# Kernel tuning notes

Hardware: AMD Instinct MI355X
Metric: run time of the kernel (lower is better)

The kernel has to match this reference:

```python
import jax, jax.numpy as jnp
import numpy as np

B, M = 512, 256
IN1, IN2, IN3 = 20000, 15000, 20000


def setup_inputs() -> dict:
    key = jax.random.key(0)
    ks = jax.random.split(key, 16)
    s1, s2, s3, s4 = 1.0 / np.sqrt(IN1), 1.0 / np.sqrt(IN2), 1.0 / np.sqrt(IN3), 1.0 / np.sqrt(4 * M)
    return {
        "expression": jax.random.normal(ks[0], (B, IN1), jnp.float32),
        "mutation": jax.random.uniform(ks[1], (B, IN2), jnp.float32),
        "cna": jax.random.normal(ks[2], (B, IN3), jnp.float32),
        "We_x": jax.random.normal(ks[3], (M, IN1), jnp.float32) * s1,
        "We_y": jax.random.normal(ks[4], (M, IN1), jnp.float32) * s1,
        "Wm_x": jax.random.normal(ks[5], (M, IN2), jnp.float32) * s2,
        "Wm_y": jax.random.normal(ks[6], (M, IN2), jnp.float32) * s2,
        "Wc_x": jax.random.normal(ks[7], (M, IN3), jnp.float32) * s3,
        "Wc_y": jax.random.normal(ks[8], (M, IN3), jnp.float32) * s3,
        "W3e": jax.random.normal(ks[9], (1, 4 * M), jnp.float32) * s4,
        "b3e": jnp.zeros((1,), jnp.float32),
        "W3m": jax.random.normal(ks[10], (1, 4 * M), jnp.float32) * s4,
        "b3m": jnp.zeros((1,), jnp.float32),
        "W3c": jax.random.normal(ks[11], (1, 4 * M), jnp.float32) * s4,
        "b3c": jnp.zeros((1,), jnp.float32),
    }


def reference(expression, mutation, cna, We_x, We_y, Wm_x, Wm_y, Wc_x, Wc_y,
              W3e, b3e, W3m, b3m, W3c, b3c):
    def proj(x, Wx, Wy):  # (B,F) -> (B,2,M)
        return jnp.stack([x @ Wx.T, x @ Wy.T], axis=1)

    def l2norm(t):  # normalize over the 2-row axis, like torch.norm(dim=1,keepdim=True)
        return t / jnp.linalg.norm(t, axis=1, keepdims=True)

    e = l2norm(proj(expression, We_x, We_y))
    m = l2norm(proj(mutation, Wm_x, Wm_y))
    c = l2norm(proj(cna, Wc_x, Wc_y))

    energy = lambda a, b: jnp.einsum('bkm,bkn->bmn', a, b)  # (B,M,M), k=2
    E_em, E_ec, E_mc = energy(e, m), energy(e, c), energy(m, c)

    att_em = jax.nn.softmax(E_em, axis=1)                     # softmax over dim1
    att_ec = jax.nn.softmax(E_ec, axis=1)
    att_me = jnp.swapaxes(jax.nn.softmax(E_em, axis=-1), 1, 2)
    att_mc = jax.nn.softmax(E_mc, axis=-1)                    # double permute cancels
    att_ce = jnp.swapaxes(jax.nn.softmax(E_ec, axis=-1), 1, 2)
    att_cm = jnp.swapaxes(jax.nn.softmax(E_mc, axis=-1), 1, 2)

    w = lambda x, a: jnp.einsum('bkm,bmn->bkn', x, a)  # (B,2,M)
    e_feat = jnp.concatenate([w(e, att_em), w(e, att_ec)], axis=1).reshape(-1, 4 * e.shape[-1])
    m_feat = jnp.concatenate([w(m, att_me), w(m, att_mc)], axis=1).reshape(-1, 4 * e.shape[-1])
    c_feat = jnp.concatenate([w(c, att_ce), w(c, att_cm)], axis=1).reshape(-1, 4 * e.shape[-1])

    head = lambda f, W, b: jnp.squeeze(jax.nn.sigmoid(f @ W.T + b))
    return head(e_feat, W3e, b3e), head(m_feat, W3m, b3m), head(c_feat, W3c, b3c)
```

## Files before the change

### kernel.cpp

```cpp
#include <hip/hip_runtime.h>
#include <hip/hip_bf16.h>

typedef short short8 __attribute__((ext_vector_type(8)));
typedef float float4v __attribute__((ext_vector_type(4)));

#define TK 32
#define MAXSPLIT 20
#define APAD 40

__device__ __forceinline__ unsigned int pack2bf(float a, float b) {
    unsigned int r;
    asm("v_cvt_pk_bf16_f32 %0, %1, %2" : "=v"(r) : "v"(a), "v"(b));
    return r;
}

__global__ __launch_bounds__(512, 2) void gemm_kernel(
    const float* __restrict__ Ae, const float* __restrict__ Am, const float* __restrict__ Ac,
    const float* __restrict__ Wex, const float* __restrict__ Wey,
    const float* __restrict__ Wmx, const float* __restrict__ Wmy,
    const float* __restrict__ Wcx, const float* __restrict__ Wcy,
    float* __restrict__ part, int nsplit)
{
    int nb = gridDim.x;
    int per = nb >> 3;
    int bid = blockIdx.x;
    int job = (bid & 7) * per + (bid >> 3);

    int mod = job / (4 * nsplit);
    int rem = job - mod * 4 * nsplit;
    int split = rem >> 2;
    int t2 = rem & 3;
    int ti = t2 >> 1, tj = t2 & 1;

    const float* A; const float* Wx; const float* Wy; int K;
    if (mod == 0)      { A = Ae; Wx = Wex; Wy = Wey; K = 20000; }
    else if (mod == 1) { A = Am; Wx = Wmx; Wy = Wmy; K = 15000; }
    else               { A = Ac; Wx = Wcx; Wy = Wcy; K = 20000; }

    int chunk = ((K + nsplit * TK - 1) / (nsplit * TK)) * TK;
    int kstart = split * chunk;
    int kend = kstart + chunk; if (kend > K) kend = K;
    int nstep = (kend - kstart + TK - 1) / TK;

    const float* Abase = A + (size_t)(ti * 256) * K;
    const float* Wbase = (tj == 0) ? Wx : Wy;

    __shared__ unsigned short As[2][256][APAD];
    __shared__ unsigned short Bs[2][256][APAD];

    int tid = threadIdx.x;
    int lane = tid & 63, w = tid >> 6;
    int wr = (w & 3) * 64;
    int wc = (w >> 2) * 128;
    int q = lane >> 4, r16 = lane & 15, q8 = q * 8;

    int ra0 = tid >> 3;
    int ca  = (tid & 7) * 4;

    float4v ar[4], br[4];
    auto loadAB = [&](int k0) {
        int k = k0 + ca; if (k > K - 4) k = K - 4;
        #pragma unroll
        for (int i = 0; i < 4; ++i) {
            ar[i] = *(const float4v*)(Abase + (size_t)(ra0 + i * 64) * K + k);
            br[i] = *(const float4v*)(Wbase + (size_t)(ra0 + i * 64) * K + k);
        }
    };
    auto storeAB = [&](int buf, int k0, bool tail) {
        bool kill = tail && (k0 + ca >= kend);
        #pragma unroll
        for (int i = 0; i < 4; ++i) {
            float4v va = ar[i], vb = br[i];
            if (kill) { va = (float4v){0.f,0.f,0.f,0.f}; vb = (float4v){0.f,0.f,0.f,0.f}; }
            uint2 pa, pb;
            pa.x = pack2bf(va[0], va[1]);
            pa.y = pack2bf(va[2], va[3]);
            pb.x = pack2bf(vb[0], vb[1]);
            pb.y = pack2bf(vb[2], vb[3]);
            *(uint2*)&As[buf][ra0 + i * 64][ca] = pa;
            *(uint2*)&Bs[buf][ra0 + i * 64][ca] = pb;
        }
    };

    float4v acc[4][8];
    #pragma unroll
    for (int a = 0; a < 4; ++a)
        #pragma unroll
        for (int b = 0; b < 8; ++b)
            acc[a][b] = (float4v){0.f, 0.f, 0.f, 0.f};

    auto computeStep = [&](int buf) {
        short8 fa[4], fb[8];
        #pragma unroll
        for (int a = 0; a < 4; ++a)
            fa[a] = *(const short8*)&As[buf][wr + a * 16 + r16][q8];
        #pragma unroll
        for (int b = 0; b < 8; ++b)
            fb[b] = *(const short8*)&Bs[buf][wc + b * 16 + r16][q8];
        #pragma unroll
        for (int a = 0; a < 4; ++a)
            #pragma unroll
            for (int b = 0; b < 8; ++b)
                acc[a][b] = __builtin_amdgcn_mfma_f32_16x16x32_bf16(fa[a], fb[b], acc[a][b], 0, 0, 0);
    };

    loadAB(kstart);
    storeAB(0, kstart, kstart + TK > kend);

    for (int s = 0; s < nstep; ++s) {
        int cur = s & 1;
        int k1 = kstart + (s + 1) * TK;
        bool more = (s + 1 < nstep);
        if (more) loadAB(k1);
        __syncthreads();
        computeStep(cur);
        if (more) storeAB(cur ^ 1, k1, k1 + TK > kend);
    }

    float* pbase = part + (size_t)((mod * 4 + t2) * nsplit + split) * 65536;
    #pragma unroll
    for (int a = 0; a < 4; ++a)
        #pragma unroll
        for (int b = 0; b < 8; ++b)
            #pragma unroll
            for (int r = 0; r < 4; ++r) {
                int row = wr + a * 16 + q * 4 + r;
                int col = wc + b * 16 + r16;
                pbase[row * 256 + col] = acc[a][b][r];
            }
}

__global__ void reduce_kernel(const float* __restrict__ part, float* __restrict__ P,
                              float* __restrict__ headacc, int nsplit)
{
    int gid = blockIdx.x * 256 + threadIdx.x;
    if (gid < 1536) headacc[gid] = 0.f;
    int mod = gid >> 18;
    int rem = gid & 262143;
    int b = rem >> 9, j = rem & 511;
    int ti = b >> 8, r = b & 255, tj = j >> 8, c = j & 255;
    int t2 = ti * 2 + tj;
    const float* src = part + (size_t)((mod * 4 + t2) * nsplit) * 65536 + r * 256 + c;
    float s = 0.f;
    for (int k = 0; k < nsplit; ++k) s += src[(size_t)k * 65536];
    P[gid] = s;
}

__global__ __launch_bounds__(256) void pairs_kernel(
    const float* __restrict__ P, float* __restrict__ headacc,
    const float* __restrict__ W3e, const float* __restrict__ W3m, const float* __restrict__ W3c)
{
    int b = blockIdx.x / 3, pair = blockIdx.x % 3;
    int t = threadIdx.x;
    __shared__ float2 Pn[256], Qn[256];
    __shared__ float Rinv[256];
    __shared__ float red[4];

    int pm = (pair == 2) ? 1 : 0;
    int qm = (pair == 0) ? 1 : 2;
    const float* prow = P + pm * 262144 + b * 512;
    const float* qrow = P + qm * 262144 + b * 512;

    float px = prow[t], py = prow[256 + t];
    float ip = rsqrtf(px * px + py * py);
    Pn[t] = (float2){px * ip, py * ip};
    float qx = qrow[t], qy = qrow[256 + t];
    float iq = rsqrtf(qx * qx + qy * qy);
    Qn[t] = (float2){qx * iq, qy * iq};
    __syncthreads();

    const float L2E = 1.4426950408889634f;

    float pxr = Pn[t].x * L2E, pyr = Pn[t].y * L2E;
    float rs = 0.f, rqx = 0.f, rqy = 0.f;
    #pragma unroll 4
    for (int j = 0; j < 256; ++j) {
        float2 qv = Qn[j];
        float x = exp2f(fmaf(pyr, qv.y, pxr * qv.x));
        rs += x;
        rqx = fmaf(qv.x, x, rqx);
        rqy = fmaf(qv.y, x, rqy);
    }
    float rinv = 1.f / rs;
    Rinv[t] = rinv;
    float Fq0 = rqx * rinv, Fq1 = rqy * rinv;

    const float* WR; int hR, offR;
    if (pair == 0)      { WR = W3m; hR = 1; offR = 0; }
    else if (pair == 1) { WR = W3c; hR = 2; offR = 0; }
    else                { WR = W3c; hR = 2; offR = 512; }
    float v = Fq0 * WR[offR + t] + Fq1 * WR[offR + 256 + t];
    #pragma unroll
    for (int o = 32; o > 0; o >>= 1) v += __shfl_down(v, o, 64);
    if ((t & 63) == 0) red[t >> 6] = v;
    __syncthreads();
    if (t == 0) atomicAdd(&headacc[b * 3 + hR], red[0] + red[1] + red[2] + red[3]);
    __syncthreads();

    float qxr = Qn[t].x * L2E, qyr = Qn[t].y * L2E;
    float cs = 0.f, cpx = 0.f, cpy = 0.f;
    if (pair < 2) {
        #pragma unroll 4
        for (int i = 0; i < 256; ++i) {
            float2 pv = Pn[i];
            float x = exp2f(fmaf(qyr, pv.y, qxr * pv.x));
            cs += x;
            cpx = fmaf(pv.x, x, cpx);
            cpy = fmaf(pv.y, x, cpy);
        }
        float ci = 1.f / cs;
        cpx *= ci; cpy *= ci;
    } else {
        #pragma unroll 4
        for (int i = 0; i < 256; ++i) {
            float2 pv = Pn[i];
            float x = exp2f(fmaf(qyr, pv.y, qxr * pv.x)) * Rinv[i];
            cpx = fmaf(pv.x, x, cpx);
            cpy = fmaf(pv.y, x, cpy);
        }
    }
    const float* WC; int hC, offC;
    if (pair == 0)      { WC = W3e; hC = 0; offC = 0; }
    else if (pair == 1) { WC = W3e; hC = 0; offC = 512; }
    else                { WC = W3m; hC = 1; offC = 512; }
    float v2 = cpx * WC[offC + t] + cpy * WC[offC + 256 + t];
    #pragma unroll
    for (int o = 32; o > 0; o >>= 1) v2 += __shfl_down(v2, o, 64);
    if ((t & 63) == 0) red[t >> 6] = v2;
    __syncthreads();
    if (t == 0) atomicAdd(&headacc[b * 3 + hC], red[0] + red[1] + red[2] + red[3]);
}

__global__ void head_kernel(const float* __restrict__ headacc,
                            const float* __restrict__ b3e, const float* __restrict__ b3m,
                            const float* __restrict__ b3c, float* __restrict__ out)
{
    int i = blockIdx.x * 256 + threadIdx.x;
    if (i >= 1536) return;
    int h = i >> 9, b = i & 511;
    float bias = (h == 0) ? b3e[0] : (h == 1) ? b3m[0] : b3c[0];
    float z = headacc[b * 3 + h] + bias;
    out[i] = 1.f / (1.f + __expf(-z));
}

extern "C" void kernel_launch(void* const* d_in, const int* in_sizes, int n_in,
                              void* d_out, int out_size, void* d_ws, size_t ws_size,
                              hipStream_t stream) {
    const float* Ae  = (const float*)d_in[0];
    const float* Am  = (const float*)d_in[1];
    const float* Ac  = (const float*)d_in[2];
    const float* Wex = (const float*)d_in[3];
    const float* Wey = (const float*)d_in[4];
    const float* Wmx = (const float*)d_in[5];
    const float* Wmy = (const float*)d_in[6];
    const float* Wcx = (const float*)d_in[7];
    const float* Wcy = (const float*)d_in[8];
    const float* W3e = (const float*)d_in[9];
    const float* b3e = (const float*)d_in[10];
    const float* W3m = (const float*)d_in[11];
    const float* b3m = (const float*)d_in[12];
    const float* W3c = (const float*)d_in[13];
    const float* b3c = (const float*)d_in[14];

    size_t fixed = (size_t)786432 * 4 + 1536 * 4;
    int nsplit = 2;
    if (ws_size > fixed) {
        size_t avail = (ws_size - fixed) / ((size_t)12 * 65536 * 4);
        nsplit = (avail < MAXSPLIT) ? (int)avail : MAXSPLIT;
        if (nsplit < 2) nsplit = 2;
    }
    nsplit &= ~1;

    float* part    = (float*)d_ws;
    float* P       = part + (size_t)12 * nsplit * 65536;
    float* headacc = P + 786432;

    gemm_kernel<<<12 * nsplit, 512, 0, stream>>>(Ae, Am, Ac, Wex, Wey, Wmx, Wmy, Wcx, Wcy,
                                                 part, nsplit);
    reduce_kernel<<<3072, 256, 0, stream>>>(part, P, headacc, nsplit);
    pairs_kernel<<<1536, 256, 0, stream>>>(P, headacc, W3e, W3m, W3c);
    head_kernel<<<6, 256, 0, stream>>>(headacc, b3e, b3m, b3c, (float*)d_out);
}
```

Measured before the change: 337.4 us.

## Stage fp32 tiles via direct global-to-LDS loads with XOR swizzle

Replaces the register-staged global load, bf16 pack and LDS store with `global_load_lds` 16-byte transfers. These write fp32 tiles straight into an XOR-swizzled shared buffer. The bf16 conversion and tail zero-masking move into the fragment load before the MFMAs, and blocks with an empty K range now exit early. The aim is to free VGPRs and overlap the next tile's transfer with compute. In exchange, shared memory per block doubles to fp32 tiles, which likely rules out two blocks per CU. Conversion work is also repeated by every wave that reads a row, and the early exit leaves those partial slots unwritten.

```diff
diff --git a/kernel.cpp b/kernel.cpp
--- a/kernel.cpp
+++ b/kernel.cpp
@@ -6,7 +6,13 @@
 
 #define TK 32
 #define MAXSPLIT 20
-#define APAD 40
+
+typedef const __attribute__((address_space(1))) void* gas_ptr;
+typedef __attribute__((address_space(3))) void* las_ptr;
+
+__device__ __forceinline__ void dma16(const float* g, float* l) {
+    __builtin_amdgcn_global_load_lds((gas_ptr)g, (las_ptr)l, 16, 0, 0);
+}
 
 __device__ __forceinline__ unsigned int pack2bf(float a, float b) {
     unsigned int r;
@@ -40,45 +46,31 @@
     int chunk = ((K + nsplit * TK - 1) / (nsplit * TK)) * TK;
     int kstart = split * chunk;
     int kend = kstart + chunk; if (kend > K) kend = K;
+    if (kstart >= kend) return;
     int nstep = (kend - kstart + TK - 1) / TK;
 
     const float* Abase = A + (size_t)(ti * 256) * K;
     const float* Wbase = (tj == 0) ? Wx : Wy;
 
-    __shared__ unsigned short As[2][256][APAD];
-    __shared__ unsigned short Bs[2][256][APAD];
+    __shared__ float As[2][8192];
+    __shared__ float Bs[2][8192];
 
     int tid = threadIdx.x;
     int lane = tid & 63, w = tid >> 6;
     int wr = (w & 3) * 64;
     int wc = (w >> 2) * 128;
     int q = lane >> 4, r16 = lane & 15, q8 = q * 8;
-
-    int ra0 = tid >> 3;
-    int ca  = (tid & 7) * 4;
-
-    float4v ar[4], br[4];
-    auto loadAB = [&](int k0) {
-        int k = k0 + ca; if (k > K - 4) k = K - 4;
+    int lrow = lane >> 3, l8 = lane & 7;
+
+    auto dmaAll = [&](int buf, int k0) {
         #pragma unroll
         for (int i = 0; i < 4; ++i) {
-            ar[i] = *(const float4v*)(Abase + (size_t)(ra0 + i * 64) * K + k);
-            br[i] = *(const float4v*)(Wbase + (size_t)(ra0 + i * 64) * K + k);
-        }
-    };
-    auto storeAB = [&](int buf, int k0, bool tail) {
-        bool kill = tail && (k0 + ca >= kend);
-        #pragma unroll
-        for (int i = 0; i < 4; ++i) {
-            float4v va = ar[i], vb = br[i];
-            if (kill) { va = (float4v){0.f,0.f,0.f,0.f}; vb = (float4v){0.f,0.f,0.f,0.f}; }
-            uint2 pa, pb;
-            pa.x = pack2bf(va[0], va[1]);
-            pa.y = pack2bf(va[2], va[3]);
-            pb.x = pack2bf(vb[0], vb[1]);
-            pb.y = pack2bf(vb[2], vb[3]);
-            *(uint2*)&As[buf][ra0 + i * 64][ca] = pa;
-            *(uint2*)&Bs[buf][ra0 + i * 64][ca] = pb;
+            int c = i * 8 + w;
+            int r = c * 8 + lrow;
+            int g = l8 ^ (r & 7);
+            int k = k0 + g * 4; if (k > K - 4) k = K - 4;
+            dma16(Abase + (size_t)r * K + k, &As[buf][c * 256]);
+            dma16(Wbase + (size_t)r * K + k, &Bs[buf][c * 256]);
         }
     };
 
@@ -89,14 +81,42 @@
         for (int b = 0; b < 8; ++b)
             acc[a][b] = (float4v){0.f, 0.f, 0.f, 0.f};
 
-    auto computeStep = [&](int buf) {
+    auto computeStep = [&](int buf, int k0, bool tail) {
+        bool z0 = false, z1 = false;
+        if (tail) { z0 = (k0 + q8 >= kend); z1 = (k0 + q8 + 4 >= kend); }
         short8 fa[4], fb[8];
         #pragma unroll
-        for (int a = 0; a < 4; ++a)
-            fa[a] = *(const short8*)&As[buf][wr + a * 16 + r16][q8];
-        #pragma unroll
-        for (int b = 0; b < 8; ++b)
-            fb[b] = *(const short8*)&Bs[buf][wc + b * 16 + r16][q8];
+        for (int a = 0; a < 4; ++a) {
+            int r = wr + a * 16 + r16;
+            int rx = r & 7;
+            const float* rowp = &As[buf][r * 32];
+            float4v g0 = *(const float4v*)(rowp + (((2 * q)     ^ rx) * 4));
+            float4v g1 = *(const float4v*)(rowp + (((2 * q + 1) ^ rx) * 4));
+            if (z0) g0 = (float4v){0.f, 0.f, 0.f, 0.f};
+            if (z1) g1 = (float4v){0.f, 0.f, 0.f, 0.f};
+            union { unsigned int u[4]; short8 s; } pk;
+            pk.u[0] = pack2bf(g0[0], g0[1]);
+            pk.u[1] = pack2bf(g0[2], g0[3]);
+            pk.u[2] = pack2bf(g1[0], g1[1]);
+            pk.u[3] = pack2bf(g1[2], g1[3]);
+            fa[a] = pk.s;
+        }
+        #pragma unroll
+        for (int b = 0; b < 8; ++b) {
+            int r = wc + b * 16 + r16;
+            int rx = r & 7;
+            const float* rowp = &Bs[buf][r * 32];
+            float4v g0 = *(const float4v*)(rowp + (((2 * q)     ^ rx) * 4));
+            float4v g1 = *(const float4v*)(rowp + (((2 * q + 1) ^ rx) * 4));
+            if (z0) g0 = (float4v){0.f, 0.f, 0.f, 0.f};
+            if (z1) g1 = (float4v){0.f, 0.f, 0.f, 0.f};
+            union { unsigned int u[4]; short8 s; } pk;
+            pk.u[0] = pack2bf(g0[0], g0[1]);
+            pk.u[1] = pack2bf(g0[2], g0[3]);
+            pk.u[2] = pack2bf(g1[0], g1[1]);
+            pk.u[3] = pack2bf(g1[2], g1[3]);
+            fb[b] = pk.s;
+        }
         #pragma unroll
         for (int a = 0; a < 4; ++a)
             #pragma unroll
@@ -104,17 +124,16 @@
                 acc[a][b] = __builtin_amdgcn_mfma_f32_16x16x32_bf16(fa[a], fb[b], acc[a][b], 0, 0, 0);
     };
 
-    loadAB(kstart);
-    storeAB(0, kstart, kstart + TK > kend);
+    dmaAll(0, kstart);
 
     for (int s = 0; s < nstep; ++s) {
         int cur = s & 1;
-        int k1 = kstart + (s + 1) * TK;
+        int k0 = kstart + s * TK;
         bool more = (s + 1 < nstep);
-        if (more) loadAB(k1);
         __syncthreads();
-        computeStep(cur);
-        if (more) storeAB(cur ^ 1, k1, k1 + TK > kend);
+        if (more) dmaAll(cur ^ 1, k0 + TK);
+        __builtin_amdgcn_sched_barrier(0);
+        computeStep(cur, k0, k0 + TK > kend);
     }
 
     float* pbase = part + (size_t)((mod * 4 + t2) * nsplit + split) * 65536;
```

Measured after the change: 352.7 us. 4.5% more time.
